# Optimization experiments

Hardware: AMD Instinct MI355X
Metric: run time of the kernel (lower is better)

Reference implementation:

```python
import jax, jax.numpy as jnp
import numpy as np

N_QUBITS = 7
N_LAYERS = 5
DIM = 2 ** N_QUBITS  # 128


def _apply_1q(state, U, q):
    """Apply single-qubit gate U ((2,2) shared or (B,2,2) per-sample) on wire q.
    state: (B, 2,2,2,2,2,2,2), wire 0 = most significant axis (PennyLane order)."""
    state = jnp.moveaxis(state, 1 + q, -1)
    if U.ndim == 2:
        state = state @ U.T
    else:
        state = jnp.einsum('bij,b...j->b...i', U, state)
    return jnp.moveaxis(state, -1, 1 + q)


def _apply_cnot(state, c, t):
    state = jnp.moveaxis(state, (1 + c, 1 + t), (-2, -1))
    new = jnp.stack([state[..., 0, :], state[..., 1, ::-1]], axis=-2)
    return jnp.moveaxis(new, (-2, -1), (1 + c, 1 + t))


def _rot_matrix(phi, theta, omega):
    # PennyLane Rot(phi, theta, omega) = RZ(omega) @ RY(theta) @ RZ(phi)
    c = jnp.cos(theta / 2)
    s = jnp.sin(theta / 2)
    ep = jnp.exp(-0.5j * (phi + omega))
    em = jnp.exp(0.5j * (phi - omega))
    row0 = jnp.stack([ep * c, -em * s])
    row1 = jnp.stack([jnp.conj(em) * s, jnp.conj(ep) * c])
    return jnp.stack([row0, row1]).astype(jnp.complex64)


def _simulate(x, qweights):
    B = x.shape[0]
    state = jnp.zeros((B, DIM), jnp.complex64).at[:, 0].set(1.0)
    state = state.reshape((B,) + (2,) * N_QUBITS)
    # AngleEmbedding rotation='Y': RY(x_q) on wire q, per-sample angles
    c = jnp.cos(x / 2)
    s = jnp.sin(x / 2)
    for q in range(N_QUBITS):
        U = jnp.stack([jnp.stack([c[:, q], -s[:, q]], -1),
                       jnp.stack([s[:, q], c[:, q]], -1)], -2).astype(jnp.complex64)
        state = _apply_1q(state, U, q)
    # StronglyEntanglingLayers: Rot on each wire, then ring of CNOTs with range r
    for l in range(N_LAYERS):
        r = l % (N_QUBITS - 1) + 1
        for q in range(N_QUBITS):
            state = _apply_1q(state, _rot_matrix(qweights[l, q, 0], qweights[l, q, 1], qweights[l, q, 2]), q)
        for q in range(N_QUBITS):
            state = _apply_cnot(state, q, (q + r) % N_QUBITS)
    # expval(PauliZ(q)) for each wire
    probs = (state.real ** 2 + state.imag ** 2).reshape(B, DIM)
    idx = jnp.arange(DIM)
    bits = (idx[None, :] >> (N_QUBITS - 1 - jnp.arange(N_QUBITS))[:, None]) & 1  # (7,128)
    signs = (1 - 2 * bits).astype(probs.dtype)
    return probs @ signs.T  # (B, 7)


def setup_inputs() -> dict:
    key = jax.random.key(0)
    ks = jax.random.split(key, 6)
    B, n_classes = 32768, 22
    x = jax.random.normal(ks[0], (B, N_QUBITS), dtype=jnp.float32)
    qweights = jax.random.uniform(ks[1], (N_LAYERS, N_QUBITS, 3), dtype=jnp.float32,
                                  minval=0.0, maxval=2.0 * np.pi)
    W1 = jax.random.normal(ks[2], (16, N_QUBITS), dtype=jnp.float32) / np.sqrt(N_QUBITS)
    b1 = jax.random.normal(ks[3], (16,), dtype=jnp.float32) * 0.01
    W2 = jax.random.normal(ks[4], (n_classes, 16), dtype=jnp.float32) / 4.0
    b2 = jax.random.normal(ks[5], (n_classes,), dtype=jnp.float32) * 0.01
    return {"x": x, "qweights": qweights, "W1": W1, "b1": b1, "W2": W2, "b2": b2}


def reference(x, qweights, W1, b1, W2, b2):
    q_out = _simulate(x, qweights)              # (B, 7) real expvals
    h = jax.nn.relu(q_out @ W1.T + b1)          # (B, 16)
    # Dropout(p=0.3) is identity in eval mode
    logits = h @ W2.T + b2                      # (B, 22)
    return logits
```

## Files before the change

### kernel.cpp

```cpp
#include <hip/hip_runtime.h>
#include <math.h>

#define DIM 128

typedef __attribute__((ext_vector_type(8))) short bf16x8;
typedef __attribute__((ext_vector_type(4))) float f32x4;

static __device__ __forceinline__ unsigned short f2bf(float v) {
  unsigned u = __float_as_uint(v);
  unsigned r = (u + 0x7FFFu + ((u >> 16) & 1u)) >> 16;
  return (unsigned short)r;
}
static __device__ __forceinline__ float bf2f(unsigned short u) {
  return __uint_as_float(((unsigned)u) << 16);
}

__global__ __launch_bounds__(256) void build_unitary_k(
    const float* __restrict__ qw, unsigned short* __restrict__ Bhi,
    unsigned short* __restrict__ Blo) {
  __shared__ float gm[35][8];
  const int tid = threadIdx.x;

  if (tid < 35) {
    const float phi = qw[tid * 3 + 0];
    const float th  = qw[tid * 3 + 1];
    const float om  = qw[tid * 3 + 2];
    float sh, ch; sincosf(0.5f * th, &sh, &ch);
    const float a = 0.5f * (phi + om);
    const float b = 0.5f * (phi - om);
    float sa, ca; sincosf(a, &sa, &ca);
    float sb, cb; sincosf(b, &sb, &cb);
    gm[tid][0] =  ca * ch;  gm[tid][1] = -sa * ch;
    gm[tid][2] = -cb * sh;  gm[tid][3] = -sb * sh;
    gm[tid][4] =  cb * sh;  gm[tid][5] = -sb * sh;
    gm[tid][6] =  ca * ch;  gm[tid][7] =  sa * ch;
  }
  __syncthreads();

  const int lane = tid & 63;
  const int k    = blockIdx.x * 4 + (tid >> 6);

  float rl = (k == lane)      ? 1.f : 0.f;
  float rh = (k == lane + 64) ? 1.f : 0.f;
  float il = 0.f, ih = 0.f;

  for (int l = 0; l < 5; ++l) {
    const int r = l % 6 + 1;
    for (int q = 0; q < 7; ++q) {
      const float* g = gm[l * 7 + q];
      const float g0 = g[0], g1 = g[1], g2 = g[2], g3 = g[3];
      const float g4 = g[4], g5 = g[5], g6 = g[6], g7 = g[7];
      if (q == 0) {
        const float nrl = g0 * rl - g1 * il + g2 * rh - g3 * ih;
        const float nil = g0 * il + g1 * rl + g2 * ih + g3 * rh;
        const float nrh = g4 * rl - g5 * il + g6 * rh - g7 * ih;
        const float nih = g4 * il + g5 * rl + g6 * ih + g7 * rh;
        rl = nrl; il = nil; rh = nrh; ih = nih;
      } else {
        const int m = 1 << (6 - q);
        const int bit = (lane & m) ? 1 : 0;
        const float prl = __shfl_xor(rl, m), pil = __shfl_xor(il, m);
        const float prh = __shfl_xor(rh, m), pih = __shfl_xor(ih, m);
        const float udr = bit ? g6 : g0, udi = bit ? g7 : g1;
        const float uor = bit ? g4 : g2, uoi = bit ? g5 : g3;
        const float nrl = udr * rl - udi * il + uor * prl - uoi * pil;
        const float nil = udr * il + udi * rl + uor * pil + uoi * prl;
        const float nrh = udr * rh - udi * ih + uor * prh - uoi * pih;
        const float nih = udr * ih + udi * rh + uor * pih + uoi * prh;
        rl = nrl; il = nil; rh = nrh; ih = nih;
      }
    }
    for (int q = 0; q < 7; ++q) {
      const int tg = (q + r) % 7;
      if (q == 0) {
        const int mt = 1 << (6 - tg);
        const float prh = __shfl_xor(rh, mt), pih = __shfl_xor(ih, mt);
        rh = prh; ih = pih;
      } else if (tg == 0) {
        const int mc = 1 << (6 - q);
        const bool cb = (lane & mc) != 0;
        const float trl = cb ? rh : rl, til = cb ? ih : il;
        const float trh = cb ? rl : rh, tih = cb ? il : ih;
        rl = trl; il = til; rh = trh; ih = tih;
      } else {
        const int mc = 1 << (6 - q), mt = 1 << (6 - tg);
        const bool cb = (lane & mc) != 0;
        const float prl = __shfl_xor(rl, mt), pil = __shfl_xor(il, mt);
        const float prh = __shfl_xor(rh, mt), pih = __shfl_xor(ih, mt);
        rl = cb ? prl : rl; il = cb ? pil : il;
        rh = cb ? prh : rh; ih = cb ? pih : ih;
      }
    }
  }

  const int kt = k >> 5, kl = (k >> 3) & 3, e = k & 7;
  {
    const float vals[4] = {rl, rh, il, ih};
    #pragma unroll
    for (int t = 0; t < 4; ++t) {
      const int n = lane + t * 64;
      const int off = (((n >> 4) * 4 + kt) * 64 + kl * 16 + (n & 15)) * 8 + e;
      const unsigned short h = f2bf(vals[t]);
      Bhi[off] = h;
      Blo[off] = f2bf(vals[t] - bf2f(h));
    }
  }
}

__global__ __launch_bounds__(512, 4) void vqc_mlp_k(
    const float* __restrict__ x,
    const unsigned short* __restrict__ Bhi, const unsigned short* __restrict__ Blo,
    const float* __restrict__ W1, const float* __restrict__ b1,
    const float* __restrict__ W2, const float* __restrict__ b2,
    float* __restrict__ out) {
  __shared__ float smem[4608];
  unsigned short* Ahi = (unsigned short*)smem;
  unsigned short* Alo = (unsigned short*)(smem + 2176);
  float* qaP = smem;
  float* QA  = smem + 2304;

  const int tid  = threadIdx.x;
  const int lane = tid & 63;
  const int w    = tid >> 6;
  const int s0   = blockIdx.x * 32;

  const bf16x8* __restrict__ Bh8 = (const bf16x8*)Bhi;
  const bf16x8* __restrict__ Bl8 = (const bf16x8*)Blo;
  bf16x8 bh[2][4], bl[2][4];
  #pragma unroll
  for (int t = 0; t < 2; ++t) {
    const int ct = w + t * 8;
    #pragma unroll
    for (int kt = 0; kt < 4; ++kt) {
      bh[t][kt] = Bh8[(ct * 4 + kt) * 64 + lane];
      bl[t][kt] = Bl8[(ct * 4 + kt) * 64 + lane];
    }
  }

  {
    const int sam = tid >> 4;
    const int ko  = tid & 15;
    const float* xp = x + (s0 + sam) * 7;
    float cq[7], sq[7];
    #pragma unroll
    for (int q = 0; q < 7; ++q) __sincosf(0.5f * xp[q], &sq[q], &cq[q]);
    float sv[8];
    sv[0] = ((ko & 8) ? sq[0] : cq[0]) * ((ko & 4) ? sq[1] : cq[1]) *
            ((ko & 2) ? sq[2] : cq[2]) * ((ko & 1) ? sq[3] : cq[3]);
    #pragma unroll
    for (int q = 4; q < 7; ++q) {
      const int cnt = 1 << (q - 4);
      #pragma unroll
      for (int t2 = cnt - 1; t2 >= 0; --t2) {
        const float v = sv[t2];
        sv[2 * t2 + 1] = v * sq[q];
        sv[2 * t2]     = v * cq[q];
      }
    }
    bf16x8 h8, l8;
    #pragma unroll
    for (int e = 0; e < 8; ++e) {
      const unsigned short h = f2bf(sv[e]);
      h8[e] = (short)h;
      l8[e] = (short)f2bf(sv[e] - bf2f(h));
    }
    *(bf16x8*)&Ahi[sam * 136 + ko * 8] = h8;
    *(bf16x8*)&Alo[sam * 136 + ko * 8] = l8;
  }
  __syncthreads();

  f32x4 acc00 = {0.f, 0.f, 0.f, 0.f};
  f32x4 acc01 = {0.f, 0.f, 0.f, 0.f};
  f32x4 acc10 = {0.f, 0.f, 0.f, 0.f};
  f32x4 acc11 = {0.f, 0.f, 0.f, 0.f};
  const int r0 = (lane & 15) * 136;
  const int r1 = (16 + (lane & 15)) * 136;
  const int kloff = (lane >> 4) * 8;
  #pragma unroll
  for (int kt = 0; kt < 4; ++kt) {
    const int ko2 = kt * 32 + kloff;
    const bf16x8 ah0 = *(const bf16x8*)&Ahi[r0 + ko2];
    const bf16x8 al0 = *(const bf16x8*)&Alo[r0 + ko2];
    const bf16x8 ah1 = *(const bf16x8*)&Ahi[r1 + ko2];
    const bf16x8 al1 = *(const bf16x8*)&Alo[r1 + ko2];
    acc00 = __builtin_amdgcn_mfma_f32_16x16x32_bf16(bh[0][kt], ah0, acc00, 0, 0, 0);
    acc01 = __builtin_amdgcn_mfma_f32_16x16x32_bf16(bh[1][kt], ah0, acc01, 0, 0, 0);
    acc10 = __builtin_amdgcn_mfma_f32_16x16x32_bf16(bh[0][kt], ah1, acc10, 0, 0, 0);
    acc11 = __builtin_amdgcn_mfma_f32_16x16x32_bf16(bh[1][kt], ah1, acc11, 0, 0, 0);
    acc00 = __builtin_amdgcn_mfma_f32_16x16x32_bf16(bl[0][kt], ah0, acc00, 0, 0, 0);
    acc01 = __builtin_amdgcn_mfma_f32_16x16x32_bf16(bl[1][kt], ah0, acc01, 0, 0, 0);
    acc10 = __builtin_amdgcn_mfma_f32_16x16x32_bf16(bl[0][kt], ah1, acc10, 0, 0, 0);
    acc11 = __builtin_amdgcn_mfma_f32_16x16x32_bf16(bl[1][kt], ah1, acc11, 0, 0, 0);
    acc00 = __builtin_amdgcn_mfma_f32_16x16x32_bf16(bh[0][kt], al0, acc00, 0, 0, 0);
    acc01 = __builtin_amdgcn_mfma_f32_16x16x32_bf16(bh[1][kt], al0, acc01, 0, 0, 0);
    acc10 = __builtin_amdgcn_mfma_f32_16x16x32_bf16(bh[0][kt], al1, acc10, 0, 0, 0);
    acc11 = __builtin_amdgcn_mfma_f32_16x16x32_bf16(bh[1][kt], al1, acc11, 0, 0, 0);
  }

  const int sg0 = (w >> 2) & 1, sg1 = (w >> 1) & 1, sg2 = w & 1;
  float qv7[2][7];
  #pragma unroll
  for (int st = 0; st < 2; ++st) {
    const f32x4 yr = (st == 0) ? acc00 : acc10;
    const f32x4 yi = (st == 0) ? acc01 : acc11;
    const float p0 = yr[0] * yr[0] + yi[0] * yi[0];
    const float p1 = yr[1] * yr[1] + yi[1] * yi[1];
    const float p2 = yr[2] * yr[2] + yi[2] * yi[2];
    const float p3 = yr[3] * yr[3] + yi[3] * yi[3];
    const float t  = p0 + p1 + p2 + p3;
    const float d5 = p0 + p1 - p2 - p3;
    const float d6 = p0 - p1 + p2 - p3;
    const float t16 = __shfl_xor(t, 16);
    const float a   = t + t16;
    const float b4  = (lane & 16) ? (t16 - t) : (t - t16);
    const float a32 = __shfl_xor(a, 32);
    const float T   = a + a32;
    const float D3  = (lane & 32) ? (a32 - a) : (a - a32);
    const float D4  = b4 + __shfl_xor(b4, 32);
    const float d5a = d5 + __shfl_xor(d5, 16);
    const float D5  = d5a + __shfl_xor(d5a, 32);
    const float d6a = d6 + __shfl_xor(d6, 16);
    const float D6  = d6a + __shfl_xor(d6a, 32);
    qv7[st][0] = sg0 ? -T : T;
    qv7[st][1] = sg1 ? -T : T;
    qv7[st][2] = sg2 ? -T : T;
    qv7[st][3] = D3; qv7[st][4] = D4; qv7[st][5] = D5; qv7[st][6] = D6;
  }
  __syncthreads();

  if (lane < 16) {
    #pragma unroll
    for (int st = 0; st < 2; ++st) {
      const int base = w * 288 + (st * 16 + lane) * 9;
      #pragma unroll
      for (int q = 0; q < 7; ++q) qaP[base + q] = qv7[st][q];
    }
  }
  __syncthreads();

  if (tid < 224) {
    const int q = tid >> 5, s = tid & 31;
    float acc = 0.f;
    #pragma unroll
    for (int wv = 0; wv < 8; ++wv) acc += qaP[wv * 288 + s * 9 + q];
    QA[s * 8 + q] = acc;
  }
  __syncthreads();

  if (tid < 352) {
    const int s  = tid / 11;
    const int oo = tid - s * 11;
    float qv[7];
    #pragma unroll
    for (int q = 0; q < 7; ++q) qv[q] = QA[s * 8 + q];
    float h[16];
    #pragma unroll
    for (int k = 0; k < 16; ++k) {
      float a2 = b1[k];
      #pragma unroll
      for (int q = 0; q < 7; ++q) a2 += W1[k * 7 + q] * qv[q];
      h[k] = fmaxf(a2, 0.f);
    }
    #pragma unroll
    for (int oi = 0; oi < 2; ++oi) {
      const int o = oo + oi * 11;
      float lg2 = b2[o];
      #pragma unroll
      for (int k = 0; k < 16; ++k) lg2 += W2[o * 16 + k] * h[k];
      out[(s0 + s) * 22 + o] = lg2;
    }
  }
}

extern "C" void kernel_launch(void* const* d_in, const int* in_sizes, int n_in,
                              void* d_out, int out_size, void* d_ws, size_t ws_size,
                              hipStream_t stream) {
  const float* x  = (const float*)d_in[0];
  const float* qw = (const float*)d_in[1];
  const float* W1 = (const float*)d_in[2];
  const float* b1 = (const float*)d_in[3];
  const float* W2 = (const float*)d_in[4];
  const float* b2 = (const float*)d_in[5];
  float* out = (float*)d_out;
  unsigned short* Bhi = (unsigned short*)d_ws;
  unsigned short* Blo = Bhi + 128 * 256;

  const int B = in_sizes[0] / 7;

  build_unitary_k<<<32, 256, 0, stream>>>(qw, Bhi, Blo);

  vqc_mlp_k<<<B / 32, 512, 0, stream>>>(x, Bhi, Blo, W1, b1, W2, b2, out);
}
```

Baseline: 82.37 us.

## Replace split-bf16 triple MFMA with single fp16 MFMA and double samples per block

Drops the hi/lo bf16 split of both the unitary and the state vectors and uses a single fp16 MFMA per tile, cutting matrix work to a third. Each block now handles 64 samples instead of 32, so each wave runs four sample subtiles. The unitary fragments are loaded inside the k-loop instead of being held in registers, and the MLP epilogue thread mapping changes to 8 threads per sample. Accuracy now rests on fp16's 11-bit mantissa rather than emulated near-fp32 precision, which may be too loose for tolerance checks.

```diff
diff --git a/kernel.cpp b/kernel.cpp
--- a/kernel.cpp
+++ b/kernel.cpp
@@ -3,21 +3,18 @@
 
 #define DIM 128
 
-typedef __attribute__((ext_vector_type(8))) short bf16x8;
+typedef __attribute__((ext_vector_type(8))) _Float16 f16x8;
 typedef __attribute__((ext_vector_type(4))) float f32x4;
 
-static __device__ __forceinline__ unsigned short f2bf(float v) {
-  unsigned u = __float_as_uint(v);
-  unsigned r = (u + 0x7FFFu + ((u >> 16) & 1u)) >> 16;
-  return (unsigned short)r;
-}
-static __device__ __forceinline__ float bf2f(unsigned short u) {
-  return __uint_as_float(((unsigned)u) << 16);
+static __device__ __forceinline__ unsigned short f2h(float v) {
+  _Float16 hv = (_Float16)v;
+  unsigned short u;
+  __builtin_memcpy(&u, &hv, 2);
+  return u;
 }
 
 __global__ __launch_bounds__(256) void build_unitary_k(
-    const float* __restrict__ qw, unsigned short* __restrict__ Bhi,
-    unsigned short* __restrict__ Blo) {
+    const float* __restrict__ qw, unsigned short* __restrict__ Bf) {
   __shared__ float gm[35][8];
   const int tid = threadIdx.x;
 
@@ -100,56 +97,39 @@
     for (int t = 0; t < 4; ++t) {
       const int n = lane + t * 64;
       const int off = (((n >> 4) * 4 + kt) * 64 + kl * 16 + (n & 15)) * 8 + e;
-      const unsigned short h = f2bf(vals[t]);
-      Bhi[off] = h;
-      Blo[off] = f2bf(vals[t] - bf2f(h));
+      Bf[off] = f2h(vals[t]);
     }
   }
 }
 
 __global__ __launch_bounds__(512, 4) void vqc_mlp_k(
-    const float* __restrict__ x,
-    const unsigned short* __restrict__ Bhi, const unsigned short* __restrict__ Blo,
+    const float* __restrict__ x, const unsigned short* __restrict__ Bf,
     const float* __restrict__ W1, const float* __restrict__ b1,
     const float* __restrict__ W2, const float* __restrict__ b2,
     float* __restrict__ out) {
-  __shared__ float smem[4608];
-  unsigned short* Ahi = (unsigned short*)smem;
-  unsigned short* Alo = (unsigned short*)(smem + 2176);
+  __shared__ float smem[5120];
+  unsigned short* Ahf = (unsigned short*)smem;
   float* qaP = smem;
-  float* QA  = smem + 2304;
+  float* QA  = smem + 4608;
 
   const int tid  = threadIdx.x;
   const int lane = tid & 63;
   const int w    = tid >> 6;
-  const int s0   = blockIdx.x * 32;
-
-  const bf16x8* __restrict__ Bh8 = (const bf16x8*)Bhi;
-  const bf16x8* __restrict__ Bl8 = (const bf16x8*)Blo;
-  bf16x8 bh[2][4], bl[2][4];
-  #pragma unroll
-  for (int t = 0; t < 2; ++t) {
-    const int ct = w + t * 8;
-    #pragma unroll
-    for (int kt = 0; kt < 4; ++kt) {
-      bh[t][kt] = Bh8[(ct * 4 + kt) * 64 + lane];
-      bl[t][kt] = Bl8[(ct * 4 + kt) * 64 + lane];
-    }
-  }
+  const int s0   = blockIdx.x * 64;
 
   {
-    const int sam = tid >> 4;
-    const int ko  = tid & 15;
+    const int sam = tid >> 3;
+    const int ko  = tid & 7;
     const float* xp = x + (s0 + sam) * 7;
     float cq[7], sq[7];
     #pragma unroll
     for (int q = 0; q < 7; ++q) __sincosf(0.5f * xp[q], &sq[q], &cq[q]);
-    float sv[8];
-    sv[0] = ((ko & 8) ? sq[0] : cq[0]) * ((ko & 4) ? sq[1] : cq[1]) *
-            ((ko & 2) ? sq[2] : cq[2]) * ((ko & 1) ? sq[3] : cq[3]);
-    #pragma unroll
-    for (int q = 4; q < 7; ++q) {
-      const int cnt = 1 << (q - 4);
+    float sv[16];
+    sv[0] = ((ko & 4) ? sq[0] : cq[0]) * ((ko & 2) ? sq[1] : cq[1]) *
+            ((ko & 1) ? sq[2] : cq[2]);
+    #pragma unroll
+    for (int q = 3; q < 7; ++q) {
+      const int cnt = 1 << (q - 3);
       #pragma unroll
       for (int t2 = cnt - 1; t2 >= 0; --t2) {
         const float v = sv[t2];
@@ -157,52 +137,47 @@
         sv[2 * t2]     = v * cq[q];
       }
     }
-    bf16x8 h8, l8;
+    f16x8 h8a, h8b;
     #pragma unroll
     for (int e = 0; e < 8; ++e) {
-      const unsigned short h = f2bf(sv[e]);
-      h8[e] = (short)h;
-      l8[e] = (short)f2bf(sv[e] - bf2f(h));
-    }
-    *(bf16x8*)&Ahi[sam * 136 + ko * 8] = h8;
-    *(bf16x8*)&Alo[sam * 136 + ko * 8] = l8;
-  }
-  __syncthreads();
-
-  f32x4 acc00 = {0.f, 0.f, 0.f, 0.f};
-  f32x4 acc01 = {0.f, 0.f, 0.f, 0.f};
-  f32x4 acc10 = {0.f, 0.f, 0.f, 0.f};
-  f32x4 acc11 = {0.f, 0.f, 0.f, 0.f};
-  const int r0 = (lane & 15) * 136;
-  const int r1 = (16 + (lane & 15)) * 136;
+      h8a[e] = (_Float16)sv[e];
+      h8b[e] = (_Float16)sv[8 + e];
+    }
+    *(f16x8*)&Ahf[sam * 136 + ko * 16]     = h8a;
+    *(f16x8*)&Ahf[sam * 136 + ko * 16 + 8] = h8b;
+  }
+  __syncthreads();
+
+  const f16x8* __restrict__ Bf8 = (const f16x8*)Bf;
+  const int boff0 = (w * 4) * 64 + lane;
+  const int boff1 = ((w + 8) * 4) * 64 + lane;
+  f32x4 accR[4], accI[4];
+  #pragma unroll
+  for (int st = 0; st < 4; ++st) {
+    accR[st] = (f32x4){0.f, 0.f, 0.f, 0.f};
+    accI[st] = (f32x4){0.f, 0.f, 0.f, 0.f};
+  }
   const int kloff = (lane >> 4) * 8;
+  const int csub  = lane & 15;
   #pragma unroll
   for (int kt = 0; kt < 4; ++kt) {
+    const f16x8 bh0 = Bf8[boff0 + kt * 64];
+    const f16x8 bh1 = Bf8[boff1 + kt * 64];
     const int ko2 = kt * 32 + kloff;
-    const bf16x8 ah0 = *(const bf16x8*)&Ahi[r0 + ko2];
-    const bf16x8 al0 = *(const bf16x8*)&Alo[r0 + ko2];
-    const bf16x8 ah1 = *(const bf16x8*)&Ahi[r1 + ko2];
-    const bf16x8 al1 = *(const bf16x8*)&Alo[r1 + ko2];
-    acc00 = __builtin_amdgcn_mfma_f32_16x16x32_bf16(bh[0][kt], ah0, acc00, 0, 0, 0);
-    acc01 = __builtin_amdgcn_mfma_f32_16x16x32_bf16(bh[1][kt], ah0, acc01, 0, 0, 0);
-    acc10 = __builtin_amdgcn_mfma_f32_16x16x32_bf16(bh[0][kt], ah1, acc10, 0, 0, 0);
-    acc11 = __builtin_amdgcn_mfma_f32_16x16x32_bf16(bh[1][kt], ah1, acc11, 0, 0, 0);
-    acc00 = __builtin_amdgcn_mfma_f32_16x16x32_bf16(bl[0][kt], ah0, acc00, 0, 0, 0);
-    acc01 = __builtin_amdgcn_mfma_f32_16x16x32_bf16(bl[1][kt], ah0, acc01, 0, 0, 0);
-    acc10 = __builtin_amdgcn_mfma_f32_16x16x32_bf16(bl[0][kt], ah1, acc10, 0, 0, 0);
-    acc11 = __builtin_amdgcn_mfma_f32_16x16x32_bf16(bl[1][kt], ah1, acc11, 0, 0, 0);
-    acc00 = __builtin_amdgcn_mfma_f32_16x16x32_bf16(bh[0][kt], al0, acc00, 0, 0, 0);
-    acc01 = __builtin_amdgcn_mfma_f32_16x16x32_bf16(bh[1][kt], al0, acc01, 0, 0, 0);
-    acc10 = __builtin_amdgcn_mfma_f32_16x16x32_bf16(bh[0][kt], al1, acc10, 0, 0, 0);
-    acc11 = __builtin_amdgcn_mfma_f32_16x16x32_bf16(bh[1][kt], al1, acc11, 0, 0, 0);
+    #pragma unroll
+    for (int st = 0; st < 4; ++st) {
+      const f16x8 ah = *(const f16x8*)&Ahf[(st * 16 + csub) * 136 + ko2];
+      accR[st] = __builtin_amdgcn_mfma_f32_16x16x32_f16(bh0, ah, accR[st], 0, 0, 0);
+      accI[st] = __builtin_amdgcn_mfma_f32_16x16x32_f16(bh1, ah, accI[st], 0, 0, 0);
+    }
   }
 
   const int sg0 = (w >> 2) & 1, sg1 = (w >> 1) & 1, sg2 = w & 1;
-  float qv7[2][7];
+  float qv7[4][7];
   #pragma unroll
-  for (int st = 0; st < 2; ++st) {
-    const f32x4 yr = (st == 0) ? acc00 : acc10;
-    const f32x4 yi = (st == 0) ? acc01 : acc11;
+  for (int st = 0; st < 4; ++st) {
+    const f32x4 yr = accR[st];
+    const f32x4 yi = accI[st];
     const float p0 = yr[0] * yr[0] + yi[0] * yi[0];
     const float p1 = yr[1] * yr[1] + yi[1] * yi[1];
     const float p2 = yr[2] * yr[2] + yi[2] * yi[2];
@@ -230,26 +205,26 @@
 
   if (lane < 16) {
     #pragma unroll
-    for (int st = 0; st < 2; ++st) {
-      const int base = w * 288 + (st * 16 + lane) * 9;
+    for (int st = 0; st < 4; ++st) {
+      const int base = w * 576 + (st * 16 + lane) * 9;
       #pragma unroll
       for (int q = 0; q < 7; ++q) qaP[base + q] = qv7[st][q];
     }
   }
   __syncthreads();
 
-  if (tid < 224) {
-    const int q = tid >> 5, s = tid & 31;
+  if (tid < 448) {
+    const int q = tid >> 6, s = tid & 63;
     float acc = 0.f;
     #pragma unroll
-    for (int wv = 0; wv < 8; ++wv) acc += qaP[wv * 288 + s * 9 + q];
+    for (int wv = 0; wv < 8; ++wv) acc += qaP[wv * 576 + s * 9 + q];
     QA[s * 8 + q] = acc;
   }
   __syncthreads();
 
-  if (tid < 352) {
-    const int s  = tid / 11;
-    const int oo = tid - s * 11;
+  {
+    const int s  = tid >> 3;
+    const int t8 = tid & 7;
     float qv[7];
     #pragma unroll
     for (int q = 0; q < 7; ++q) qv[q] = QA[s * 8 + q];
@@ -262,12 +237,14 @@
       h[k] = fmaxf(a2, 0.f);
     }
     #pragma unroll
-    for (int oi = 0; oi < 2; ++oi) {
-      const int o = oo + oi * 11;
-      float lg2 = b2[o];
-      #pragma unroll
-      for (int k = 0; k < 16; ++k) lg2 += W2[o * 16 + k] * h[k];
-      out[(s0 + s) * 22 + o] = lg2;
+    for (int oi = 0; oi < 3; ++oi) {
+      const int o = t8 + oi * 8;
+      if (o < 22) {
+        float lg2 = b2[o];
+        #pragma unroll
+        for (int k = 0; k < 16; ++k) lg2 += W2[o * 16 + k] * h[k];
+        out[(s0 + s) * 22 + o] = lg2;
+      }
     }
   }
 }
@@ -282,12 +259,11 @@
   const float* W2 = (const float*)d_in[4];
   const float* b2 = (const float*)d_in[5];
   float* out = (float*)d_out;
-  unsigned short* Bhi = (unsigned short*)d_ws;
-  unsigned short* Blo = Bhi + 128 * 256;
+  unsigned short* Bf = (unsigned short*)d_ws;
 
   const int B = in_sizes[0] / 7;
 
-  build_unitary_k<<<32, 256, 0, stream>>>(qw, Bhi, Blo);
-
-  vqc_mlp_k<<<B / 32, 512, 0, stream>>>(x, Bhi, Blo, W1, b1, W2, b2, out);
-}
+  build_unitary_k<<<32, 256, 0, stream>>>(qw, Bf);
+
+  vqc_mlp_k<<<B / 64, 512, 0, stream>>>(x, Bf, W1, b1, W2, b2, out);
+}
```

Result: faster. 77.72 us (-5.6%).
